# Kernel optimization log

Measured on AMD Instinct MI355X. Metric: run time of the kernel, lower is better.

Reference implementation:

```python
import jax, jax.numpy as jnp
import numpy as np

D_MODEL = 1024
D_STATE = 16
D_CONV = 4
EXPAND = 2
D_INNER = EXPAND * D_MODEL  # 2048
DT_RANK = 16  # per source: list(range(1,17))[-1] since d_inner >= 16
BATCH = 2
SEQ = 1024


def setup_inputs() -> dict:
    key = jax.random.key(0)
    ks = jax.random.split(key, 8)
    s = 0.02
    return {
        "x": jax.random.normal(ks[0], (BATCH, SEQ, D_MODEL), jnp.float32),
        # torch Linear convention: weight [out, in]
        "in_proj_w": jax.random.normal(ks[1], (2 * D_INNER, D_MODEL), jnp.float32) * s,
        "in_proj_b": jnp.zeros((2 * D_INNER,), jnp.float32),
        # depthwise conv: [d_inner, 1, d_conv]
        "conv_w": jax.random.normal(ks[2], (D_INNER, 1, D_CONV), jnp.float32) * s,
        "conv_b": jnp.zeros((D_INNER,), jnp.float32),
        "x_proj_w": jax.random.normal(ks[3], (DT_RANK + 2 * D_STATE, D_INNER), jnp.float32) * s,
        "x_proj_b": jnp.zeros((DT_RANK + 2 * D_STATE,), jnp.float32),
        "dt_proj_w": jax.random.normal(ks[4], (D_INNER, DT_RANK), jnp.float32) * s,
        "dt_proj_b": jnp.zeros((D_INNER,), jnp.float32),
        "A_log": jnp.log(jnp.broadcast_to(jnp.arange(1, D_STATE + 1, dtype=jnp.float32), (D_INNER, D_STATE))),
        "D": jnp.ones((D_INNER,), jnp.float32),
        "out_proj_w": jax.random.normal(ks[5], (D_MODEL, D_INNER), jnp.float32) * s,
        "out_proj_b": jnp.zeros((D_MODEL,), jnp.float32),
    }


def _mamba(x, in_proj_w, in_proj_b, conv_w, conv_b, x_proj_w, x_proj_b,
           dt_proj_w, dt_proj_b, A_log, D, out_proj_w, out_proj_b):
    # in_proj and split into x / res branches
    x_and_res = x @ in_proj_w.T + in_proj_b                       # [B, L, 2*d_inner]
    xs, res = jnp.split(x_and_res, [D_INNER], axis=-1)
    # causal depthwise conv: left-pad d_conv-1, which matches padding=d_conv-1 then [:, :, :l]
    xc = jnp.transpose(xs, (0, 2, 1))                             # [B, d_inner, L]
    xc = jax.lax.conv_general_dilated(
        xc, conv_w, window_strides=(1,), padding=[(D_CONV - 1, 0)],
        feature_group_count=D_INNER, dimension_numbers=("NCH", "OIH", "NCH"))
    xc = xc + conv_b[None, :, None]
    xs = jax.nn.silu(jnp.transpose(xc, (0, 2, 1)))                # [B, L, d_inner]

    # SSM input-dependent parameters
    x_dbl = xs @ x_proj_w.T + x_proj_b                            # [B, L, dt_rank + 2n]
    dlt, Bm, Cm = jnp.split(x_dbl, [DT_RANK, DT_RANK + D_STATE], axis=-1)
    delta = jax.nn.softplus(dlt @ dt_proj_w.T + dt_proj_b)        # [B, L, d_inner]
    A = -jnp.exp(A_log)                                           # [d_inner, n]

    # selective scan over time
    def step(h, inputs):
        d_t, x_t, b_t, c_t = inputs                               # [B,d],[B,d],[B,n],[B,n]
        dA = jnp.exp(d_t[:, :, None] * A)                         # [B, d, n]
        h = dA * h + (d_t * x_t)[:, :, None] * b_t[:, None, :]    # [B, d, n]
        y_t = jnp.einsum("bdn,bn->bd", h, c_t)                   # [B, d]
        return h, y_t

    h0 = jnp.zeros((xs.shape[0], D_INNER, D_STATE), xs.dtype)
    seq_inputs = (jnp.moveaxis(delta, 1, 0), jnp.moveaxis(xs, 1, 0),
                  jnp.moveaxis(Bm, 1, 0), jnp.moveaxis(Cm, 1, 0))
    _, ys = jax.lax.scan(step, h0, seq_inputs)                    # ys: [L, B, d_inner]
    y = jnp.moveaxis(ys, 0, 1) + xs * D                           # skip term D

    y = y * jax.nn.silu(res)                                      # gating
    return y @ out_proj_w.T + out_proj_b                          # [B, L, d_model]


def reference(x, in_proj_w, in_proj_b, conv_w, conv_b, x_proj_w, x_proj_b,
              dt_proj_w, dt_proj_b, A_log, D, out_proj_w, out_proj_b):
    return _mamba(x, in_proj_w, in_proj_b, conv_w, conv_b, x_proj_w, x_proj_b,
                  dt_proj_w, dt_proj_b, A_log, D, out_proj_w, out_proj_b)
```

## Files before the change

kernel.cpp:

```cpp
#include <hip/hip_runtime.h>

#define D_MODEL 1024
#define D_STATE 16
#define D_CONV  4
#define D_INNER 2048
#define DT_RANK 16
#define BATCH   2
#define SEQ     1024
#define M_ROWS  (BATCH*SEQ)
#define CHUNK   32
#define NCHUNK  (SEQ/CHUNK)

typedef __bf16 bf16x8 __attribute__((ext_vector_type(8)));
typedef float  f32x4  __attribute__((ext_vector_type(4)));

__device__ __forceinline__ unsigned short f2bf(float f) {
  unsigned u = __float_as_uint(f);
  u += 0x7fffu + ((u >> 16) & 1u);
  return (unsigned short)(u >> 16);
}

__device__ __forceinline__ float sigmoid_fast(float v) {
  return 1.f / (1.f + __expf(-v));
}

__device__ __forceinline__ float softplus_f(float s) {
  return (s > 20.f) ? s : __logf(1.f + __expf(s));
}

__device__ __forceinline__ void gll16(const void* g, void* l) {
  __builtin_amdgcn_global_load_lds(
      (const __attribute__((address_space(1))) unsigned int*)g,
      (__attribute__((address_space(3))) unsigned int*)l, 16, 0, 0);
}

__device__ __forceinline__ void storeC(float v, float* p)          { *p = v; }
__device__ __forceinline__ void storeC(float v, unsigned short* p) { *p = f2bf(v); }

__global__ __launch_bounds__(256) void cast_all_kernel(
    const float* __restrict__ x, const float* __restrict__ w1, const float* __restrict__ w2,
    const float* __restrict__ xpw,
    unsigned short* __restrict__ xbf, unsigned short* __restrict__ w1bf,
    unsigned short* __restrict__ w2bf, unsigned short* __restrict__ xpwbf) {
  const int N0 = (M_ROWS * D_MODEL) / 4;
  const int N1 = (2 * D_INNER * D_MODEL) / 4;
  const int N2 = (D_MODEL * D_INNER) / 4;
  int i = blockIdx.x * 256 + threadIdx.x;
  const float* src; unsigned short* dst; int off;
  if (i < N0)                 { src = x;   dst = xbf;   off = i; }
  else if (i < N0 + N1)       { src = w1;  dst = w1bf;  off = i - N0; }
  else if (i < N0 + N1 + N2)  { src = w2;  dst = w2bf;  off = i - N0 - N1; }
  else                        { src = xpw; dst = xpwbf; off = i - N0 - N1 - N2; }
  float4 v = *(const float4*)(src + (size_t)off * 4);
  ushort4 o;
  o.x = f2bf(v.x); o.y = f2bf(v.y); o.z = f2bf(v.z); o.w = f2bf(v.w);
  *(ushort4*)(dst + (size_t)off * 4) = o;
}

template<int BM, typename CT>
__global__ __launch_bounds__(256) void gemm_gll(
    const __bf16* __restrict__ A, const __bf16* __restrict__ B,
    const float* __restrict__ bias, CT* __restrict__ C,
    int M, int N, int K) {
  constexpr int MR = BM / 32;
  __shared__ __bf16 As[BM][32];
  __shared__ __bf16 Bs[128][32];
  const int tid  = threadIdx.x;
  const int lane = tid & 63;
  const int w    = tid >> 6;
  const int wr   = w >> 1, wc = w & 1;
  const int rowBase = blockIdx.y * BM;
  const int colBase = blockIdx.x * 128;

  f32x4 acc[MR][4];
  #pragma unroll
  for (int i = 0; i < MR; ++i)
    #pragma unroll
    for (int j = 0; j < 4; ++j) { f32x4 z = {0.f,0.f,0.f,0.f}; acc[i][j] = z; }

  const int srow = lane >> 2;
  const int sk   = (lane & 3) * 8;
  const int fr   = lane & 15;
  const int fk   = (lane >> 4) * 8;

  for (int k0 = 0; k0 < K; k0 += 32) {
    #pragma unroll
    for (int i = 0; i < BM / 64; ++i) {
      const int r0 = w * (BM / 4) + i * 16;
      gll16(A + (size_t)(rowBase + r0 + srow) * K + k0 + sk, &As[r0][0]);
    }
    #pragma unroll
    for (int i = 0; i < 2; ++i) {
      const int r0 = w * 32 + i * 16;
      gll16(B + (size_t)(colBase + r0 + srow) * K + k0 + sk, &Bs[r0][0]);
    }
    __syncthreads();

    bf16x8 af[MR], bfr[4];
    #pragma unroll
    for (int mm = 0; mm < MR; ++mm)
      af[mm] = *(const bf16x8*)&As[wr * (BM / 2) + mm * 16 + fr][fk];
    #pragma unroll
    for (int nn = 0; nn < 4; ++nn)
      bfr[nn] = *(const bf16x8*)&Bs[wc * 64 + nn * 16 + fr][fk];
    #pragma unroll
    for (int mm = 0; mm < MR; ++mm)
      #pragma unroll
      for (int nn = 0; nn < 4; ++nn)
        acc[mm][nn] = __builtin_amdgcn_mfma_f32_16x16x32_bf16(af[mm], bfr[nn], acc[mm][nn], 0, 0, 0);
    __syncthreads();
  }

  #pragma unroll
  for (int nn = 0; nn < 4; ++nn) {
    int col = colBase + wc * 64 + nn * 16 + fr;
    float bv = bias[col];
    #pragma unroll
    for (int mm = 0; mm < MR; ++mm) {
      int row0 = rowBase + wr * (BM / 2) + mm * 16 + (lane >> 4) * 4;
      #pragma unroll
      for (int r = 0; r < 4; ++r)
        storeC(acc[mm][nn][r] + bv, &C[(size_t)(row0 + r) * N + col]);
    }
  }
}

__global__ __launch_bounds__(256) void conv_silu_kernel(
    const unsigned short* __restrict__ xar, const float* __restrict__ cw,
    const float* __restrict__ cb, unsigned short* __restrict__ xsbf) {
  int idx = blockIdx.x * 256 + threadIdx.x;
  int m  = idx >> 8;
  int d8 = (idx & 255) << 3;
  int t  = m & (SEQ - 1);
  const __bf16* xarb = (const __bf16*)xar;

  float4 cwl[8];
  const float4* cw4 = (const float4*)cw;
  #pragma unroll
  for (int e = 0; e < 8; ++e) cwl[e] = cw4[d8 + e];

  float acc[8];
  #pragma unroll
  for (int e = 0; e < 8; ++e) acc[e] = cb[d8 + e];

  #pragma unroll
  for (int j = 0; j < 4; ++j) {
    int tt = t - 3 + j;
    if (tt < 0) continue;
    bf16x8 v = *(const bf16x8*)&xarb[(size_t)(m - 3 + j) * (2 * D_INNER) + d8];
    const float* cj = (const float*)cwl;
    #pragma unroll
    for (int e = 0; e < 8; ++e)
      acc[e] += (float)v[e] * cj[e * 4 + j];
  }
  unsigned short o[8];
  #pragma unroll
  for (int e = 0; e < 8; ++e) {
    float s = acc[e] * sigmoid_fast(acc[e]);
    o[e] = f2bf(s);
  }
  *(ushort4*)&xsbf[(size_t)m * D_INNER + d8]     = *(ushort4*)&o[0];
  *(ushort4*)&xsbf[(size_t)m * D_INNER + d8 + 4] = *(ushort4*)&o[4];
}

__global__ __launch_bounds__(256) void xproj_mfma(
    const __bf16* __restrict__ A, const __bf16* __restrict__ B,
    const float* __restrict__ xpb,
    float* __restrict__ dlt, float* __restrict__ Bm, float* __restrict__ Cm) {
  __shared__ __bf16 As[128][40];
  __shared__ __bf16 Bs[48][40];
  const int tid  = threadIdx.x;
  const int lane = tid & 63;
  const int w    = tid >> 6;
  const int rowBase = blockIdx.x * 128;

  f32x4 acc[2][3];
  #pragma unroll
  for (int i = 0; i < 2; ++i)
    #pragma unroll
    for (int j = 0; j < 3; ++j) {
      f32x4 z = {0.f, 0.f, 0.f, 0.f};
      acc[i][j] = z;
    }

  const int sr = tid >> 2;
  const int ss = (tid & 3) * 8;
  const int fr = lane & 15;
  const int fk = (lane >> 4) * 8;

  for (int k0 = 0; k0 < D_INNER; k0 += 32) {
    const __bf16* Ap = A + (size_t)(rowBase + sr) * D_INNER + k0 + ss;
    *(bf16x8*)&As[sr][ss]      = *(const bf16x8*)Ap;
    *(bf16x8*)&As[sr + 64][ss] = *(const bf16x8*)(Ap + (size_t)64 * D_INNER);
    if (tid < 192)
      *(bf16x8*)&Bs[tid >> 2][ss] = *(const bf16x8*)(B + (size_t)(tid >> 2) * D_INNER + k0 + ss);
    __syncthreads();

    bf16x8 af[2], bfr[3];
    #pragma unroll
    for (int mm = 0; mm < 2; ++mm)
      af[mm] = *(const bf16x8*)&As[w * 32 + mm * 16 + fr][fk];
    #pragma unroll
    for (int nn = 0; nn < 3; ++nn)
      bfr[nn] = *(const bf16x8*)&Bs[nn * 16 + fr][fk];
    #pragma unroll
    for (int mm = 0; mm < 2; ++mm)
      #pragma unroll
      for (int nn = 0; nn < 3; ++nn)
        acc[mm][nn] = __builtin_amdgcn_mfma_f32_16x16x32_bf16(af[mm], bfr[nn], acc[mm][nn], 0, 0, 0);
    __syncthreads();
  }

  const int c16 = lane & 15;
  #pragma unroll
  for (int nn = 0; nn < 3; ++nn) {
    float bv = xpb[nn * 16 + c16];
    float* dst = (nn == 0) ? dlt : (nn == 1) ? Bm : Cm;
    #pragma unroll
    for (int mm = 0; mm < 2; ++mm) {
      int row0 = rowBase + w * 32 + mm * 16 + (lane >> 4) * 4;
      #pragma unroll
      for (int r = 0; r < 4; ++r)
        dst[(size_t)(row0 + r) * 16 + c16] = acc[mm][nn][r] + bv;
    }
  }
}


#define DELTA16(sarr, ttq)                                                       \
  {                                                                              \
    float4 q0 = *(const float4*)&sarr[ttq][0];                                   \
    float4 q1 = *(const float4*)&sarr[ttq][4];                                   \
    float4 q2 = *(const float4*)&sarr[ttq][8];                                   \
    float4 q3 = *(const float4*)&sarr[ttq][12];                                  \
    s += q0.x*dtwr[0] + q0.y*dtwr[1] + q0.z*dtwr[2] + q0.w*dtwr[3];              \
    s += q1.x*dtwr[4] + q1.y*dtwr[5] + q1.z*dtwr[6] + q1.w*dtwr[7];              \
    s += q2.x*dtwr[8] + q2.y*dtwr[9] + q2.z*dtwr[10] + q2.w*dtwr[11];            \
    s += q3.x*dtwr[12] + q3.y*dtwr[13] + q3.z*dtwr[14] + q3.w*dtwr[15];          \
  }

__global__ __launch_bounds__(256) void scan_phase1(
    const unsigned short* __restrict__ xsbf, const float* __restrict__ dlt,
    const float* __restrict__ Bmat, const float* __restrict__ dtw,
    const float* __restrict__ dtb, const float* __restrict__ alog,
    float* __restrict__ Hbuf, float* __restrict__ Sbuf) {
  __shared__ float dltS[CHUNK][16];
  __shared__ float BS[CHUNK][16];
  const int tid = threadIdx.x;
  const int c   = blockIdx.y;
  const int b   = blockIdx.z;
  const int d   = blockIdx.x * 256 + tid;
  const int row0 = b * SEQ + c * CHUNK;
  const __bf16* xsb16 = (const __bf16*)xsbf;
  {
    int e = tid * 2;
    int tt = e >> 4, r = e & 15;
    *(float2*)&dltS[tt][r] = *(const float2*)&dlt[(row0 + tt) * 16 + r];
    *(float2*)&BS[tt][r]   = *(const float2*)&Bmat[(row0 + tt) * 16 + r];
  }
  float dtwr[16], An[16];
  #pragma unroll
  for (int q = 0; q < 4; ++q) {
    float4 w4 = *(const float4*)&dtw[d * 16 + q * 4];
    dtwr[q*4+0] = w4.x; dtwr[q*4+1] = w4.y; dtwr[q*4+2] = w4.z; dtwr[q*4+3] = w4.w;
    float4 a4 = *(const float4*)&alog[d * 16 + q * 4];
    An[q*4+0] = -__expf(a4.x); An[q*4+1] = -__expf(a4.y);
    An[q*4+2] = -__expf(a4.z); An[q*4+3] = -__expf(a4.w);
  }
  const float dtbv = dtb[d];
  float xv[CHUNK];
  #pragma unroll
  for (int tt = 0; tt < CHUNK; ++tt)
    xv[tt] = (float)xsb16[(size_t)(row0 + tt) * D_INNER + d];
  __syncthreads();
  float dv[CHUNK];
  #pragma unroll
  for (int tt = 0; tt < CHUNK; ++tt) {
    float s = dtbv;
    DELTA16(dltS, tt);
    dv[tt] = softplus_f(s);
  }
  float h[16];
  #pragma unroll
  for (int n = 0; n < 16; ++n) h[n] = 0.f;
  float Ssum = 0.f;
  #pragma unroll
  for (int tt = 0; tt < CHUNK; ++tt) {
    const float dvt = dv[tt];
    Ssum += dvt;
    const float dvx = dvt * xv[tt];
    float4 B0 = *(const float4*)&BS[tt][0];
    float4 B1 = *(const float4*)&BS[tt][4];
    float4 B2 = *(const float4*)&BS[tt][8];
    float4 B3 = *(const float4*)&BS[tt][12];
    h[0]  = __expf(dvt*An[0])*h[0]   + dvx*B0.x;
    h[1]  = __expf(dvt*An[1])*h[1]   + dvx*B0.y;
    h[2]  = __expf(dvt*An[2])*h[2]   + dvx*B0.z;
    h[3]  = __expf(dvt*An[3])*h[3]   + dvx*B0.w;
    h[4]  = __expf(dvt*An[4])*h[4]   + dvx*B1.x;
    h[5]  = __expf(dvt*An[5])*h[5]   + dvx*B1.y;
    h[6]  = __expf(dvt*An[6])*h[6]   + dvx*B1.z;
    h[7]  = __expf(dvt*An[7])*h[7]   + dvx*B1.w;
    h[8]  = __expf(dvt*An[8])*h[8]   + dvx*B2.x;
    h[9]  = __expf(dvt*An[9])*h[9]   + dvx*B2.y;
    h[10] = __expf(dvt*An[10])*h[10] + dvx*B2.z;
    h[11] = __expf(dvt*An[11])*h[11] + dvx*B2.w;
    h[12] = __expf(dvt*An[12])*h[12] + dvx*B3.x;
    h[13] = __expf(dvt*An[13])*h[13] + dvx*B3.y;
    h[14] = __expf(dvt*An[14])*h[14] + dvx*B3.z;
    h[15] = __expf(dvt*An[15])*h[15] + dvx*B3.w;
  }
  size_t hbase = (((size_t)(b * NCHUNK + c) * D_INNER) + d) * 16;
  #pragma unroll
  for (int q = 0; q < 4; ++q) {
    float4 o = {h[q*4+0], h[q*4+1], h[q*4+2], h[q*4+3]};
    *(float4*)&Hbuf[hbase + q*4] = o;
  }
  Sbuf[((size_t)b * NCHUNK + c) * D_INNER + d] = Ssum;
}

__global__ __launch_bounds__(256) void scan_phase2(
    const float* __restrict__ alog, const float* __restrict__ Sbuf,
    float* __restrict__ Hbuf) {
  const int tid = threadIdx.x;
  const int n  = tid & 15;
  const int dl = tid >> 4;
  const int d  = blockIdx.x * 16 + dl;
  const int b  = blockIdx.y;
  const float An = -__expf(alog[d * 16 + n]);
  float h_run = 0.f;
  #pragma unroll 4
  for (int c = 0; c < NCHUNK; ++c) {
    size_t idx = (((size_t)(b * NCHUNK + c) * D_INNER) + d) * 16 + n;
    float hend = Hbuf[idx];
    float P = __expf(An * Sbuf[((size_t)b * NCHUNK + c) * D_INNER + d]);
    Hbuf[idx] = h_run;
    h_run = P * h_run + hend;
  }
}

__global__ __launch_bounds__(256) void scan_phase3(
    const unsigned short* __restrict__ xsbf, const unsigned short* __restrict__ xar,
    const float* __restrict__ dlt, const float* __restrict__ Bmat,
    const float* __restrict__ Cmat, const float* __restrict__ dtw,
    const float* __restrict__ dtb, const float* __restrict__ alog,
    const float* __restrict__ Dvec, const float* __restrict__ Hbuf,
    unsigned short* __restrict__ ybf) {
  __shared__ float dltS[CHUNK][16];
  __shared__ float BS[CHUNK][16];
  __shared__ float CS[CHUNK][16];
  const int tid = threadIdx.x;
  const int c   = blockIdx.y;
  const int b   = blockIdx.z;
  const int d   = blockIdx.x * 256 + tid;
  const int row0 = b * SEQ + c * CHUNK;
  const __bf16* xsb16 = (const __bf16*)xsbf;
  const __bf16* xarb  = (const __bf16*)xar;
  {
    int e = tid * 2;
    int tt = e >> 4, r = e & 15;
    *(float2*)&dltS[tt][r] = *(const float2*)&dlt[(row0 + tt) * 16 + r];
    *(float2*)&BS[tt][r]   = *(const float2*)&Bmat[(row0 + tt) * 16 + r];
    *(float2*)&CS[tt][r]   = *(const float2*)&Cmat[(row0 + tt) * 16 + r];
  }
  float dtwr[16], An[16];
  #pragma unroll
  for (int q = 0; q < 4; ++q) {
    float4 w4 = *(const float4*)&dtw[d * 16 + q * 4];
    dtwr[q*4+0] = w4.x; dtwr[q*4+1] = w4.y; dtwr[q*4+2] = w4.z; dtwr[q*4+3] = w4.w;
    float4 a4 = *(const float4*)&alog[d * 16 + q * 4];
    An[q*4+0] = -__expf(a4.x); An[q*4+1] = -__expf(a4.y);
    An[q*4+2] = -__expf(a4.z); An[q*4+3] = -__expf(a4.w);
  }
  const float dtbv = dtb[d];
  const float Dn   = Dvec[d];
  float h[16];
  {
    size_t hbase = (((size_t)(b * NCHUNK + c) * D_INNER) + d) * 16;
    #pragma unroll
    for (int q = 0; q < 4; ++q) {
      float4 hv = *(const float4*)&Hbuf[hbase + q*4];
      h[q*4+0] = hv.x; h[q*4+1] = hv.y; h[q*4+2] = hv.z; h[q*4+3] = hv.w;
    }
  }
  float xv[CHUNK], rv[CHUNK];
  #pragma unroll
  for (int tt = 0; tt < CHUNK; ++tt) {
    xv[tt] = (float)xsb16[(size_t)(row0 + tt) * D_INNER + d];
    rv[tt] = (float)xarb[(size_t)(row0 + tt) * (2 * D_INNER) + D_INNER + d];
  }
  __syncthreads();
  float dv[CHUNK];
  #pragma unroll
  for (int tt = 0; tt < CHUNK; ++tt) {
    float s = dtbv;
    DELTA16(dltS, tt);
    dv[tt] = softplus_f(s);
  }
  #pragma unroll
  for (int tt = 0; tt < CHUNK; ++tt) {
    const float dvt = dv[tt];
    const float dvx = dvt * xv[tt];
    float4 B0 = *(const float4*)&BS[tt][0];
    float4 B1 = *(const float4*)&BS[tt][4];
    float4 B2 = *(const float4*)&BS[tt][8];
    float4 B3 = *(const float4*)&BS[tt][12];
    float4 C0 = *(const float4*)&CS[tt][0];
    float4 C1 = *(const float4*)&CS[tt][4];
    float4 C2 = *(const float4*)&CS[tt][8];
    float4 C3 = *(const float4*)&CS[tt][12];
    float y = 0.f;
    h[0]  = __expf(dvt*An[0])*h[0]   + dvx*B0.x;  y += h[0]*C0.x;
    h[1]  = __expf(dvt*An[1])*h[1]   + dvx*B0.y;  y += h[1]*C0.y;
    h[2]  = __expf(dvt*An[2])*h[2]   + dvx*B0.z;  y += h[2]*C0.z;
    h[3]  = __expf(dvt*An[3])*h[3]   + dvx*B0.w;  y += h[3]*C0.w;
    h[4]  = __expf(dvt*An[4])*h[4]   + dvx*B1.x;  y += h[4]*C1.x;
    h[5]  = __expf(dvt*An[5])*h[5]   + dvx*B1.y;  y += h[5]*C1.y;
    h[6]  = __expf(dvt*An[6])*h[6]   + dvx*B1.z;  y += h[6]*C1.z;
    h[7]  = __expf(dvt*An[7])*h[7]   + dvx*B1.w;  y += h[7]*C1.w;
    h[8]  = __expf(dvt*An[8])*h[8]   + dvx*B2.x;  y += h[8]*C2.x;
    h[9]  = __expf(dvt*An[9])*h[9]   + dvx*B2.y;  y += h[9]*C2.y;
    h[10] = __expf(dvt*An[10])*h[10] + dvx*B2.z;  y += h[10]*C2.z;
    h[11] = __expf(dvt*An[11])*h[11] + dvx*B2.w;  y += h[11]*C2.w;
    h[12] = __expf(dvt*An[12])*h[12] + dvx*B3.x;  y += h[12]*C3.x;
    h[13] = __expf(dvt*An[13])*h[13] + dvx*B3.y;  y += h[13]*C3.y;
    h[14] = __expf(dvt*An[14])*h[14] + dvx*B3.z;  y += h[14]*C3.z;
    h[15] = __expf(dvt*An[15])*h[15] + dvx*B3.w;  y += h[15]*C3.w;
    y += xv[tt] * Dn;
    const float r = rv[tt];
    const float v = y * (r * sigmoid_fast(r));
    ybf[(size_t)(row0 + tt) * D_INNER + d] = f2bf(v);
  }
}

extern "C" void kernel_launch(void* const* d_in, const int* in_sizes, int n_in,
                              void* d_out, int out_size, void* d_ws, size_t ws_size,
                              hipStream_t stream) {
  const float* x    = (const float*)d_in[0];
  const float* ipw  = (const float*)d_in[1];
  const float* ipb  = (const float*)d_in[2];
  const float* cw   = (const float*)d_in[3];
  const float* cb   = (const float*)d_in[4];
  const float* xpw  = (const float*)d_in[5];
  const float* xpb  = (const float*)d_in[6];
  const float* dtw  = (const float*)d_in[7];
  const float* dtb  = (const float*)d_in[8];
  const float* alog = (const float*)d_in[9];
  const float* Dv   = (const float*)d_in[10];
  const float* opw  = (const float*)d_in[11];
  const float* opb  = (const float*)d_in[12];
  float* out = (float*)d_out;

  char* ws = (char*)d_ws;
  size_t off = 0;
  auto alloc = [&](size_t bytes) {
    char* p = ws + off;
    off += (bytes + 255) & ~(size_t)255;
    return p;
  };
  unsigned short* xbf   = (unsigned short*)alloc((size_t)M_ROWS * D_MODEL * 2);
  unsigned short* w1bf  = (unsigned short*)alloc((size_t)2 * D_INNER * D_MODEL * 2);
  unsigned short* w2bf  = (unsigned short*)alloc((size_t)D_MODEL * D_INNER * 2);
  unsigned short* xpwbf = (unsigned short*)alloc((size_t)48 * D_INNER * 2);
  unsigned short* xar   = (unsigned short*)alloc((size_t)M_ROWS * 2 * D_INNER * 2);
  unsigned short* xsbf  = (unsigned short*)alloc((size_t)M_ROWS * D_INNER * 2);
  float* dlt = (float*)alloc((size_t)M_ROWS * 16 * 4);
  float* Bm  = (float*)alloc((size_t)M_ROWS * 16 * 4);
  float* Cm  = (float*)alloc((size_t)M_ROWS * 16 * 4);
  unsigned short* ybf = (unsigned short*)alloc((size_t)M_ROWS * D_INNER * 2);
  if (off > ws_size) return;
  float* Hbuf = (float*)w1bf;
  float* Sbuf = (float*)xbf;

  cast_all_kernel<<<8288, 256, 0, stream>>>(x, ipw, opw, xpw, xbf, w1bf, w2bf, xpwbf);
  gemm_gll<128, unsigned short><<<dim3(4096 / 128, 2048 / 128), 256, 0, stream>>>(
      (const __bf16*)xbf, (const __bf16*)w1bf, ipb, xar, M_ROWS, 2 * D_INNER, D_MODEL);
  conv_silu_kernel<<<2048, 256, 0, stream>>>(xar, cw, cb, xsbf);
  xproj_mfma<<<M_ROWS / 128, 256, 0, stream>>>(
      (const __bf16*)xsbf, (const __bf16*)xpwbf, xpb, dlt, Bm, Cm);
  scan_phase1<<<dim3(D_INNER / 256, NCHUNK, BATCH), 256, 0, stream>>>(
      xsbf, dlt, Bm, dtw, dtb, alog, Hbuf, Sbuf);
  scan_phase2<<<dim3(D_INNER / 16, BATCH), 256, 0, stream>>>(alog, Sbuf, Hbuf);
  scan_phase3<<<dim3(D_INNER / 256, NCHUNK, BATCH), 256, 0, stream>>>(
      xsbf, xar, dlt, Bm, Cm, dtw, dtb, alog, Dv, Hbuf, ybf);
  gemm_gll<64, float><<<dim3(1024 / 128, 2048 / 64), 256, 0, stream>>>(
      (const __bf16*)ybf, (const __bf16*)w2bf, opb, out, M_ROWS, D_MODEL, D_INNER);
}
```

Baseline: 278.9 us.

## Split-K the x_proj GEMM across many blocks with atomic accumulation

The x_proj GEMM previously ran on only 16 blocks, each walking the full 2048-long K dimension. It is now split 16 ways over K with 64-row tiles, giving 512 blocks that accumulate into the delta/B/C buffers with float atomicAdd; only the first K-slice adds the bias. The output buffers are zeroed by extra blocks appended to the existing cast kernel, and tile loads now use global_load_lds. This trades a long serial K loop on a nearly idle GPU for atomic traffic and non-deterministic summation order.

```diff
diff --git a/kernel.cpp b/kernel.cpp
--- a/kernel.cpp
+++ b/kernel.cpp
@@ -10,6 +10,8 @@
 #define M_ROWS  (BATCH*SEQ)
 #define CHUNK   32
 #define NCHUNK  (SEQ/CHUNK)
+#define XP_KSPLIT 16
+#define XP_KLEN (D_INNER / XP_KSPLIT)
 
 typedef __bf16 bf16x8 __attribute__((ext_vector_type(8)));
 typedef float  f32x4  __attribute__((ext_vector_type(4)));
@@ -41,16 +43,23 @@
     const float* __restrict__ x, const float* __restrict__ w1, const float* __restrict__ w2,
     const float* __restrict__ xpw,
     unsigned short* __restrict__ xbf, unsigned short* __restrict__ w1bf,
-    unsigned short* __restrict__ w2bf, unsigned short* __restrict__ xpwbf) {
+    unsigned short* __restrict__ w2bf, unsigned short* __restrict__ xpwbf,
+    float* __restrict__ zbuf ) {
   const int N0 = (M_ROWS * D_MODEL) / 4;
   const int N1 = (2 * D_INNER * D_MODEL) / 4;
   const int N2 = (D_MODEL * D_INNER) / 4;
+  const int N3 = (48 * D_INNER) / 4;
   int i = blockIdx.x * 256 + threadIdx.x;
   const float* src; unsigned short* dst; int off;
   if (i < N0)                 { src = x;   dst = xbf;   off = i; }
   else if (i < N0 + N1)       { src = w1;  dst = w1bf;  off = i - N0; }
   else if (i < N0 + N1 + N2)  { src = w2;  dst = w2bf;  off = i - N0 - N1; }
-  else                        { src = xpw; dst = xpwbf; off = i - N0 - N1 - N2; }
+  else if (i < N0 + N1 + N2 + N3) { src = xpw; dst = xpwbf; off = i - N0 - N1 - N2; }
+  else {
+    float4 z = {0.f, 0.f, 0.f, 0.f};
+    ((float4*)zbuf)[i - N0 - N1 - N2 - N3] = z;
+    return;
+  }
   float4 v = *(const float4*)(src + (size_t)off * 4);
   ushort4 o;
   o.x = f2bf(v.x); o.y = f2bf(v.y); o.z = f2bf(v.z); o.w = f2bf(v.w);
@@ -167,62 +176,47 @@
     const __bf16* __restrict__ A, const __bf16* __restrict__ B,
     const float* __restrict__ xpb,
     float* __restrict__ dlt, float* __restrict__ Bm, float* __restrict__ Cm) {
-  __shared__ __bf16 As[128][40];
-  __shared__ __bf16 Bs[48][40];
+  __shared__ __bf16 As[64][32];
+  __shared__ __bf16 Bs[48][32];
   const int tid  = threadIdx.x;
   const int lane = tid & 63;
   const int w    = tid >> 6;
-  const int rowBase = blockIdx.x * 128;
-
-  f32x4 acc[2][3];
-  #pragma unroll
-  for (int i = 0; i < 2; ++i)
-    #pragma unroll
-    for (int j = 0; j < 3; ++j) {
-      f32x4 z = {0.f, 0.f, 0.f, 0.f};
-      acc[i][j] = z;
+  const int rowBase = blockIdx.x * 64;
+  const int kbase   = blockIdx.y * XP_KLEN;
+
+  f32x4 acc[3];
+  #pragma unroll
+  for (int j = 0; j < 3; ++j) { f32x4 z = {0.f,0.f,0.f,0.f}; acc[j] = z; }
+
+  const int srow = lane >> 2;
+  const int sk   = (lane & 3) * 8;
+  const int fr   = lane & 15;
+  const int fk   = (lane >> 4) * 8;
+
+  for (int k0 = kbase; k0 < kbase + XP_KLEN; k0 += 32) {
+    gll16(A + (size_t)(rowBase + w * 16 + srow) * D_INNER + k0 + sk, &As[w * 16][0]);
+    if (w < 3)
+      gll16(B + (size_t)(w * 16 + srow) * D_INNER + k0 + sk, &Bs[w * 16][0]);
+    __syncthreads();
+    bf16x8 af = *(const bf16x8*)&As[w * 16 + fr][fk];
+    #pragma unroll
+    for (int nn = 0; nn < 3; ++nn) {
+      bf16x8 bv = *(const bf16x8*)&Bs[nn * 16 + fr][fk];
+      acc[nn] = __builtin_amdgcn_mfma_f32_16x16x32_bf16(af, bv, acc[nn], 0, 0, 0);
     }
-
-  const int sr = tid >> 2;
-  const int ss = (tid & 3) * 8;
-  const int fr = lane & 15;
-  const int fk = (lane >> 4) * 8;
-
-  for (int k0 = 0; k0 < D_INNER; k0 += 32) {
-    const __bf16* Ap = A + (size_t)(rowBase + sr) * D_INNER + k0 + ss;
-    *(bf16x8*)&As[sr][ss]      = *(const bf16x8*)Ap;
-    *(bf16x8*)&As[sr + 64][ss] = *(const bf16x8*)(Ap + (size_t)64 * D_INNER);
-    if (tid < 192)
-      *(bf16x8*)&Bs[tid >> 2][ss] = *(const bf16x8*)(B + (size_t)(tid >> 2) * D_INNER + k0 + ss);
     __syncthreads();
-
-    bf16x8 af[2], bfr[3];
-    #pragma unroll
-    for (int mm = 0; mm < 2; ++mm)
-      af[mm] = *(const bf16x8*)&As[w * 32 + mm * 16 + fr][fk];
-    #pragma unroll
-    for (int nn = 0; nn < 3; ++nn)
-      bfr[nn] = *(const bf16x8*)&Bs[nn * 16 + fr][fk];
-    #pragma unroll
-    for (int mm = 0; mm < 2; ++mm)
-      #pragma unroll
-      for (int nn = 0; nn < 3; ++nn)
-        acc[mm][nn] = __builtin_amdgcn_mfma_f32_16x16x32_bf16(af[mm], bfr[nn], acc[mm][nn], 0, 0, 0);
-    __syncthreads();
   }
 
   const int c16 = lane & 15;
+  const float biasOn = (blockIdx.y == 0) ? 1.f : 0.f;
   #pragma unroll
   for (int nn = 0; nn < 3; ++nn) {
-    float bv = xpb[nn * 16 + c16];
+    float bv = biasOn * xpb[nn * 16 + c16];
     float* dst = (nn == 0) ? dlt : (nn == 1) ? Bm : Cm;
-    #pragma unroll
-    for (int mm = 0; mm < 2; ++mm) {
-      int row0 = rowBase + w * 32 + mm * 16 + (lane >> 4) * 4;
-      #pragma unroll
-      for (int r = 0; r < 4; ++r)
-        dst[(size_t)(row0 + r) * 16 + c16] = acc[mm][nn][r] + bv;
-    }
+    int row0 = rowBase + w * 16 + (lane >> 4) * 4;
+    #pragma unroll
+    for (int r = 0; r < 4; ++r)
+      atomicAdd(&dst[(size_t)(row0 + r) * 16 + c16], acc[nn][r] + bv);
   }
 }
 
@@ -472,11 +466,11 @@
   float* Hbuf = (float*)w1bf;
   float* Sbuf = (float*)xbf;
 
-  cast_all_kernel<<<8288, 256, 0, stream>>>(x, ipw, opw, xpw, xbf, w1bf, w2bf, xpwbf);
+  cast_all_kernel<<<8384, 256, 0, stream>>>(x, ipw, opw, xpw, xbf, w1bf, w2bf, xpwbf, dlt);
   gemm_gll<128, unsigned short><<<dim3(4096 / 128, 2048 / 128), 256, 0, stream>>>(
       (const __bf16*)xbf, (const __bf16*)w1bf, ipb, xar, M_ROWS, 2 * D_INNER, D_MODEL);
   conv_silu_kernel<<<2048, 256, 0, stream>>>(xar, cw, cb, xsbf);
-  xproj_mfma<<<M_ROWS / 128, 256, 0, stream>>>(
+  xproj_mfma<<<dim3(M_ROWS / 64, XP_KSPLIT), 256, 0, stream>>>(
       (const __bf16*)xsbf, (const __bf16*)xpwbf, xpb, dlt, Bm, Cm);
   scan_phase1<<<dim3(D_INNER / 256, NCHUNK, BATCH), 256, 0, stream>>>(
       xsbf, dlt, Bm, dtw, dtb, alog, Hbuf, Sbuf);
```

New measurement: 249.2 us. 10.7% less time.
